# Kernel tuning notes

Measured on AMD Instinct MI355X. Metric: run time of the kernel, lower is better.

## Reference

```python
import jax, jax.numpy as jnp
import numpy as np

WIN = (8, 8)        # window height, width
HEADS = 6
DIM = 192
HEAD_DIM = DIM // HEADS
SCALE = HEAD_DIM ** -0.5
ALPHA = 0.2         # leaky_relu negative slope (tf.nn.leaky_relu / keras default)


def _leaky(t):
    return jnp.where(t >= 0, t, ALPHA * t)


def _relative_position_index():
    # Faithful to the TF code: tf.meshgrid defaults to 'xy' indexing.
    wh, ww = WIN
    mh, mw = jnp.meshgrid(jnp.arange(wh), jnp.arange(ww))  # each [ww, wh] (xy)
    coords = jnp.stack([mh, mw])                           # [2, ww, wh]
    flat = coords.reshape(2, -1)                           # [2, N]
    rel = flat[:, :, None] - flat[:, None, :]              # [2, N, N]
    rel = jnp.transpose(rel, (1, 2, 0))                    # [N, N, 2]
    idx = (rel[:, :, 0] + wh - 1) * (2 * ww - 1) + (rel[:, :, 1] + ww - 1)
    return idx                                             # [N, N] int32


def setup_inputs() -> dict:
    key = jax.random.key(0)
    ks = jax.random.split(key, 6)
    B_, N, C = 4096, WIN[0] * WIN[1], DIM
    std = 0.02
    return {
        "x": jax.random.normal(ks[0], (B_, N, C), dtype=jnp.float32),
        "wq": jax.random.normal(ks[1], (C, C), dtype=jnp.float32) * (C ** -0.5),
        "bq": jnp.zeros((C,), dtype=jnp.float32),
        "wkv": jax.random.normal(ks[2], (C, 2 * C), dtype=jnp.float32) * (C ** -0.5),
        "bkv": jnp.zeros((2 * C,), dtype=jnp.float32),
        "bias_table": jax.random.normal(ks[3], ((2 * WIN[0] - 1) * (2 * WIN[1] - 1), HEADS), dtype=jnp.float32) * std,
        "proj_w": jax.random.normal(ks[4], (C, C), dtype=jnp.float32) * (C ** -0.5),
        "proj_b": jnp.zeros((C,), dtype=jnp.float32),
    }


def reference(x, wq, bq, wkv, bkv, bias_table, proj_w, proj_b):
    B_, N, C = x.shape
    H, D = HEADS, HEAD_DIM

    # QKV projections with LeakyReLU activation (as in LinearProjection)
    q = _leaky(x @ wq + bq).reshape(B_, N, H, D).transpose(0, 2, 1, 3)      # [B,H,N,D]
    kv = _leaky(x @ wkv + bkv).reshape(B_, N, 2, H, D).transpose(2, 0, 3, 1, 4)
    k, v = kv[0], kv[1]                                                      # [B,H,N,D]

    # scaled attention scores
    attn = jnp.einsum('bhnd,bhmd->bhnm', q * SCALE, k)                       # [B,H,N,N]

    # gathered relative position bias (ratio == 1 here, tf.repeat is no-op)
    idx = _relative_position_index()                                         # [N,N]
    bias = bias_table[idx]                                                   # [N,N,H]
    attn = attn + jnp.transpose(bias, (2, 0, 1))[None]                       # [B,H,N,N]

    attn = jax.nn.softmax(attn, axis=-1)
    out = jnp.einsum('bhnm,bhmd->bhnd', attn, v)                             # [B,H,N,D]
    out = out.transpose(0, 2, 1, 3).reshape(B_, N, C)
    return out @ proj_w + proj_b
```

## Files before the change

kernel.cpp:

```cpp
#include <hip/hip_runtime.h>
#include <hip/hip_bf16.h>

typedef __bf16 bf16;
typedef bf16 bf16x8 __attribute__((ext_vector_type(8)));
typedef bf16 bf16x4 __attribute__((ext_vector_type(4)));
typedef short s16x4 __attribute__((ext_vector_type(4)));
typedef float f32x4 __attribute__((ext_vector_type(4)));

#define SCALE 0.17677669529663687f

#define OFF_B 0
#define OFF_K 12800
#define OFF_V 25600
#define SMEM_ELEMS 39424

#if defined(__has_builtin)
#if __has_builtin(__builtin_amdgcn_mfma_f32_16x16x16bf16_1k)
#define HAS_MFMA16 1
#endif
#endif

__global__ void wattn_prep(const float* __restrict__ wq, const float* __restrict__ wkv,
                           const float* __restrict__ bias_table, const float* __restrict__ proj_w,
                           bf16* __restrict__ wqkvT, bf16* __restrict__ projT,
                           float* __restrict__ biasB)
{
    int t = blockIdx.x * 256 + threadIdx.x;
    if (t < 110592) {
        int n = t / 192, k = t % 192;
        float v = (n < 192) ? wq[k * 192 + n] : wkv[k * 384 + (n - 192)];
        wqkvT[t] = (bf16)v;
    } else if (t < 147456) {
        int e = t - 110592;
        int n = e / 192, k = e % 192;
        projT[e] = (bf16)proj_w[k * 192 + n];
    } else if (t < 172032) {
        int e = t - 147456;
        int h  = e >> 12;
        int mb = (e >> 8) & 15;
        int n  = (e >> 2) & 63;
        int mr = e & 3;
        int m  = mb * 4 + mr;
        int idx = ((n & 7) - (m & 7) + 7) * 15 + ((n >> 3) - (m >> 3) + 7);
        biasB[e] = bias_table[idx * 6 + h];
    }
}

__global__ __launch_bounds__(256, 2)
void wattn_main(const float* __restrict__ x, const bf16* __restrict__ wqkvT,
                const float* __restrict__ bq, const float* __restrict__ bkv,
                const bf16* __restrict__ projT, const float* __restrict__ biasB,
                const float* __restrict__ proj_b, float* __restrict__ outg, int B)
{
    __shared__ __align__(16) bf16 smem[SMEM_ELEMS];
    const int tid = threadIdx.x;
    const int li  = tid & 15;
    const int gi  = (tid >> 4) & 3;
    const int w   = tid >> 6;
    const int win = blockIdx.x;
    if (win >= B) return;

    bf16* xq = smem + OFF_B;
    bf16* kb = smem + OFF_K;
    bf16* vt = smem + OFF_V;

    const f32x4 fzero = {0.f, 0.f, 0.f, 0.f};

    {
        const float4* xg = (const float4*)(x + (size_t)win * 12288);
#pragma unroll
        for (int i = 0; i < 12; ++i) {
            float4 p = xg[i * 256 + tid];
            int f = (i * 256 + tid) * 4;
            int r = f / 192, c = f % 192;
            bf16x4 v; v[0]=(bf16)p.x; v[1]=(bf16)p.y; v[2]=(bf16)p.z; v[3]=(bf16)p.w;
            *(bf16x4*)&xq[r * 200 + c] = v;
        }
    }
    __syncthreads();

    f32x4 acc[4][9];
#pragma unroll
    for (int rt = 0; rt < 4; ++rt)
#pragma unroll
        for (int c = 0; c < 9; ++c) acc[rt][c] = fzero;
#pragma unroll
    for (int kk = 0; kk < 6; ++kk) {
        bf16x8 a[4], bw[9];
#pragma unroll
        for (int rt = 0; rt < 4; ++rt)
            a[rt] = *(const bf16x8*)&xq[(rt * 16 + li) * 200 + kk * 32 + gi * 8];
#pragma unroll
        for (int c = 0; c < 9; ++c) {
            int T = w + 4 * c;
            bw[c] = *(const bf16x8*)&wqkvT[(size_t)(T * 16 + li) * 192 + kk * 32 + gi * 8];
        }
#pragma unroll
        for (int c = 0; c < 9; ++c)
#pragma unroll
            for (int rt = 0; rt < 4; ++rt)
                acc[rt][c] = __builtin_amdgcn_mfma_f32_16x16x32_bf16(a[rt], bw[c], acc[rt][c], 0, 0, 0);
    }
    __syncthreads();

#pragma unroll
    for (int c = 0; c < 9; ++c) {
        int T = w + 4 * c;
        int n0 = T * 16;
        float bias = (n0 < 192) ? bq[n0 + li] : bkv[n0 - 192 + li];
#pragma unroll
        for (int rt = 0; rt < 4; ++rt) {
            float vv[4];
#pragma unroll
            for (int rg = 0; rg < 4; ++rg) {
                float v = acc[rt][c][rg] + bias;
                vv[rg] = (v >= 0.f) ? v : 0.2f * v;
            }
            if (T < 12) {
#pragma unroll
                for (int rg = 0; rg < 4; ++rg)
                    xq[(rt * 16 + gi * 4 + rg) * 200 + n0 + li] = (bf16)(vv[rg] * SCALE);
            } else if (T < 24) {
#pragma unroll
                for (int rg = 0; rg < 4; ++rg)
                    kb[(rt * 16 + gi * 4 + rg) * 200 + (n0 - 192) + li] = (bf16)vv[rg];
            } else {
                int cc = n0 - 384;
                int hh = cc >> 5, d0 = cc & 31;
                bf16x4 v4;
#pragma unroll
                for (int rg = 0; rg < 4; ++rg) v4[rg] = (bf16)vv[rg];
                *(bf16x4*)&vt[(hh * 32 + d0 + li) * 72 + rt * 16 + gi * 4] = v4;
            }
        }
    }
    __syncthreads();

    bf16x4 obf[3][2][2];
    for (int jj = 0; jj < 3; ++jj) {
        int job = w * 3 + jj;
        int h   = job >> 1;
        int ct0 = (job & 1) * 2;

        bf16x8 ak[4], bqf[2];
#pragma unroll
        for (int rt = 0; rt < 4; ++rt)
            ak[rt] = *(const bf16x8*)&kb[(rt * 16 + li) * 200 + h * 32 + gi * 8];
#pragma unroll
        for (int c2 = 0; c2 < 2; ++c2)
            bqf[c2] = *(const bf16x8*)&xq[((ct0 + c2) * 16 + li) * 200 + h * 32 + gi * 8];
        f32x4 s[4][2];
#pragma unroll
        for (int rt = 0; rt < 4; ++rt)
#pragma unroll
            for (int c2 = 0; c2 < 2; ++c2)
                s[rt][c2] = __builtin_amdgcn_mfma_f32_16x16x32_bf16(ak[rt], bqf[c2], fzero, 0, 0, 0);
#pragma unroll
        for (int rt = 0; rt < 4; ++rt)
#pragma unroll
            for (int c2 = 0; c2 < 2; ++c2) {
                f32x4 bv = *(const f32x4*)&biasB[h * 4096 + (rt * 4 + gi) * 256 + ((ct0 + c2) * 16 + li) * 4];
                s[rt][c2] += bv;
            }
        float rs[2];
#pragma unroll
        for (int c2 = 0; c2 < 2; ++c2) {
            float m_ = -1e30f;
#pragma unroll
            for (int rt = 0; rt < 4; ++rt)
#pragma unroll
                for (int rg = 0; rg < 4; ++rg) m_ = fmaxf(m_, s[rt][c2][rg]);
            m_ = fmaxf(m_, __shfl_xor(m_, 16));
            m_ = fmaxf(m_, __shfl_xor(m_, 32));
            float ss = 0.f;
#pragma unroll
            for (int rt = 0; rt < 4; ++rt)
#pragma unroll
                for (int rg = 0; rg < 4; ++rg) {
                    float p = __expf(s[rt][c2][rg] - m_);
                    s[rt][c2][rg] = p;
                    ss += p;
                }
            ss += __shfl_xor(ss, 16);
            ss += __shfl_xor(ss, 32);
            rs[c2] = 1.f / ss;
        }

        f32x4 o[2][2];
#pragma unroll
        for (int dt = 0; dt < 2; ++dt)
#pragma unroll
            for (int c2 = 0; c2 < 2; ++c2) o[dt][c2] = fzero;

#if defined(HAS_MFMA16)
#pragma unroll
        for (int ks = 0; ks < 4; ++ks) {
            s16x4 va[2], pb[2];
#pragma unroll
            for (int dt = 0; dt < 2; ++dt)
                va[dt] = *(const s16x4*)&vt[(h * 32 + dt * 16 + li) * 72 + ks * 16 + gi * 4];
#pragma unroll
            for (int c2 = 0; c2 < 2; ++c2) {
                bf16x4 b4;
#pragma unroll
                for (int rg = 0; rg < 4; ++rg) b4[rg] = (bf16)s[ks][c2][rg];
                pb[c2] = __builtin_bit_cast(s16x4, b4);
            }
#pragma unroll
            for (int dt = 0; dt < 2; ++dt)
#pragma unroll
                for (int c2 = 0; c2 < 2; ++c2)
                    o[dt][c2] = __builtin_amdgcn_mfma_f32_16x16x16bf16_1k(va[dt], pb[c2], o[dt][c2], 0, 0, 0);
        }
#else
#pragma unroll
        for (int c2 = 0; c2 < 2; ++c2) {
            unsigned pk[4][2];
#pragma unroll
            for (int rt = 0; rt < 4; ++rt)
#pragma unroll
                for (int pr = 0; pr < 2; ++pr) {
                    bf16 b0 = (bf16)s[rt][c2][2 * pr];
                    bf16 b1 = (bf16)s[rt][c2][2 * pr + 1];
                    unsigned short u0, u1;
                    __builtin_memcpy(&u0, &b0, 2);
                    __builtin_memcpy(&u1, &b1, 2);
                    pk[rt][pr] = (unsigned)u0 | ((unsigned)u1 << 16);
                }
#pragma unroll
            for (int ks = 0; ks < 2; ++ks) {
                union { unsigned u[4]; bf16x8 v; } bu;
#pragma unroll
                for (int p = 0; p < 4; ++p) {
                    int srcLane = li + 16 * (2 * (gi & 1) + (p >> 1));
                    unsigned vA = __shfl(pk[2 * ks][p & 1], srcLane);
                    unsigned vB = __shfl(pk[2 * ks + 1][p & 1], srcLane);
                    bu.u[p] = (gi >> 1) ? vB : vA;
                }
#pragma unroll
                for (int dt = 0; dt < 2; ++dt) {
                    bf16x8 va = *(const bf16x8*)&vt[(h * 32 + dt * 16 + li) * 72 + ks * 32 + gi * 8];
                    o[dt][c2] = __builtin_amdgcn_mfma_f32_16x16x32_bf16(va, bu.v, o[dt][c2], 0, 0, 0);
                }
            }
        }
#endif
#pragma unroll
        for (int dt = 0; dt < 2; ++dt)
#pragma unroll
            for (int c2 = 0; c2 < 2; ++c2) {
                bf16x4 v4;
#pragma unroll
                for (int rg = 0; rg < 4; ++rg) v4[rg] = (bf16)(o[dt][c2][rg] * rs[c2]);
                obf[jj][dt][c2] = v4;
            }
    }
    __syncthreads();

#pragma unroll
    for (int jj = 0; jj < 3; ++jj) {
        int job = w * 3 + jj;
        int h   = job >> 1;
        int ct0 = (job & 1) * 2;
#pragma unroll
        for (int dt = 0; dt < 2; ++dt)
#pragma unroll
            for (int c2 = 0; c2 < 2; ++c2)
                *(bf16x4*)&xq[((ct0 + c2) * 16 + li) * 200 + h * 32 + dt * 16 + gi * 4] = obf[jj][dt][c2];
    }
    __syncthreads();

    f32x4 pacc[4][3];
#pragma unroll
    for (int rt = 0; rt < 4; ++rt)
#pragma unroll
        for (int ct = 0; ct < 3; ++ct) pacc[rt][ct] = fzero;
#pragma unroll
    for (int kk = 0; kk < 6; ++kk) {
        bf16x8 a[4], bw[3];
#pragma unroll
        for (int rt = 0; rt < 4; ++rt)
            a[rt] = *(const bf16x8*)&xq[(rt * 16 + li) * 200 + kk * 32 + gi * 8];
#pragma unroll
        for (int ct = 0; ct < 3; ++ct)
            bw[ct] = *(const bf16x8*)&projT[(size_t)(w * 48 + ct * 16 + li) * 192 + kk * 32 + gi * 8];
#pragma unroll
        for (int ct = 0; ct < 3; ++ct)
#pragma unroll
            for (int rt = 0; rt < 4; ++rt)
                pacc[rt][ct] = __builtin_amdgcn_mfma_f32_16x16x32_bf16(a[rt], bw[ct], pacc[rt][ct], 0, 0, 0);
    }
    {
        float* of = (float*)(smem + OFF_K);
#pragma unroll
        for (int ct = 0; ct < 3; ++ct) {
            int n = w * 48 + ct * 16 + li;
            float pb_ = proj_b[n];
#pragma unroll
            for (int rt = 0; rt < 4; ++rt)
#pragma unroll
                for (int rg = 0; rg < 4; ++rg)
                    of[(rt * 16 + gi * 4 + rg) * 192 + n] = pacc[rt][ct][rg] + pb_;
        }
    }
    __syncthreads();

    {
        const float4* os = (const float4*)(smem + OFF_K);
        float4* og = (float4*)(outg + (size_t)win * 12288);
#pragma unroll
        for (int i = 0; i < 12; ++i)
            og[i * 256 + tid] = os[i * 256 + tid];
    }
}

extern "C" void kernel_launch(void* const* d_in, const int* in_sizes, int n_in,
                              void* d_out, int out_size, void* d_ws, size_t ws_size,
                              hipStream_t stream)
{
    const float* x          = (const float*)d_in[0];
    const float* wq         = (const float*)d_in[1];
    const float* bq         = (const float*)d_in[2];
    const float* wkv        = (const float*)d_in[3];
    const float* bkv        = (const float*)d_in[4];
    const float* bias_table = (const float*)d_in[5];
    const float* proj_w     = (const float*)d_in[6];
    const float* proj_b     = (const float*)d_in[7];
    float* out = (float*)d_out;

    int B = in_sizes[0] / (64 * 192);

    bf16*  wqkvT = (bf16*)d_ws;
    bf16*  projT = (bf16*)((char*)d_ws + 221184);
    float* biasB = (float*)((char*)d_ws + 294912);

    wattn_prep<<<672, 256, 0, stream>>>(wq, wkv, bias_table, proj_w, wqkvT, projT, biasB);

    wattn_main<<<B, 256, 0, stream>>>(x, wqkvT, bq, bkv, projT, biasB, proj_b, out, B);
}
```

Measured before the change: 238.9 us.

## Assign one head per wave with 384-thread blocks and register-resident Q/K

Each block now runs 6 waves, one per attention head. The QKV projection is computed transposed (weights as the A operand), so each wave's Q and K tiles stay in registers and feed the score MFMAs directly. Only V goes to a small per-wave LDS region, which cuts shared memory use and removes two block-wide barriers. The output projection and the coalesced store are also re-split across the 6 waves. The aim is more resident waves and less LDS traffic per window, at the cost of register pressure under the 384-thread, 3-blocks-per-CU launch bounds.

```diff
diff --git a/kernel.cpp b/kernel.cpp
--- a/kernel.cpp
+++ b/kernel.cpp
@@ -9,10 +9,8 @@
 
 #define SCALE 0.17677669529663687f
 
-#define OFF_B 0
-#define OFF_K 12800
-#define OFF_V 25600
-#define SMEM_ELEMS 39424
+#define OFF_V 12800
+#define SMEM_ELEMS 25856
 
 #if defined(__has_builtin)
 #if __has_builtin(__builtin_amdgcn_mfma_f32_16x16x16bf16_1k)
@@ -46,11 +44,28 @@
     }
 }
 
-__global__ __launch_bounds__(256, 2)
+#if !defined(HAS_MFMA16)
+__device__ __forceinline__ bf16x8 build8(bf16x4 t0, bf16x4 t1, int li, int gi) {
+    union { bf16x4 v; unsigned u[2]; } a0, a1;
+    a0.v = t0; a1.v = t1;
+    int b = li + 32 * (gi & 1);
+    unsigned l0  = __shfl(a0.u[0], b),      l1  = __shfl(a0.u[1], b);
+    unsigned l0h = __shfl(a0.u[0], b + 16), l1h = __shfl(a0.u[1], b + 16);
+    unsigned h0  = __shfl(a1.u[0], b),      h1  = __shfl(a1.u[1], b);
+    unsigned h0h = __shfl(a1.u[0], b + 16), h1h = __shfl(a1.u[1], b + 16);
+    bool hi = (gi & 2);
+    union { bf16x8 v8; unsigned u[4]; } r;
+    r.u[0] = hi ? h0 : l0;   r.u[1] = hi ? h1 : l1;
+    r.u[2] = hi ? h0h : l0h; r.u[3] = hi ? h1h : l1h;
+    return r.v8;
+}
+#endif
+
+__global__ __launch_bounds__(384, 3)
 void wattn_main(const float* __restrict__ x, const bf16* __restrict__ wqkvT,
                 const float* __restrict__ bq, const float* __restrict__ bkv,
                 const bf16* __restrict__ projT, const float* __restrict__ biasB,
-                const float* __restrict__ proj_b, float* __restrict__ outg, int B)
+                const float* __restrict__ proj_b, float* __restrict__ outg)
 {
     __shared__ __align__(16) bf16 smem[SMEM_ELEMS];
     const int tid = threadIdx.x;
@@ -58,259 +73,224 @@
     const int gi  = (tid >> 4) & 3;
     const int w   = tid >> 6;
     const int win = blockIdx.x;
-    if (win >= B) return;
-
-    bf16* xq = smem + OFF_B;
-    bf16* kb = smem + OFF_K;
-    bf16* vt = smem + OFF_V;
-
-    const f32x4 fzero = {0.f, 0.f, 0.f, 0.f};
+
+    bf16* xb = smem;
+    bf16* vt = smem + OFF_V + w * 2176;
+
+    const int srow = tid / 48, scol = tid % 48;
+    const f32x4 fz = {0.f, 0.f, 0.f, 0.f};
 
     {
         const float4* xg = (const float4*)(x + (size_t)win * 12288);
 #pragma unroll
-        for (int i = 0; i < 12; ++i) {
-            float4 p = xg[i * 256 + tid];
-            int f = (i * 256 + tid) * 4;
-            int r = f / 192, c = f % 192;
+        for (int i = 0; i < 8; ++i) {
+            float4 p = xg[(srow + 8 * i) * 48 + scol];
             bf16x4 v; v[0]=(bf16)p.x; v[1]=(bf16)p.y; v[2]=(bf16)p.z; v[3]=(bf16)p.w;
-            *(bf16x4*)&xq[r * 200 + c] = v;
-        }
-    }
-    __syncthreads();
-
-    f32x4 acc[4][9];
-#pragma unroll
-    for (int rt = 0; rt < 4; ++rt)
-#pragma unroll
-        for (int c = 0; c < 9; ++c) acc[rt][c] = fzero;
+            *(bf16x4*)&xb[(srow + 8 * i) * 200 + scol * 4] = v;
+        }
+    }
+    __syncthreads();
+
+    f32x4 acc[6][4];
+#pragma unroll
+    for (int j = 0; j < 6; ++j)
+#pragma unroll
+        for (int c = 0; c < 4; ++c) acc[j][c] = fz;
 #pragma unroll
     for (int kk = 0; kk < 6; ++kk) {
-        bf16x8 a[4], bw[9];
-#pragma unroll
-        for (int rt = 0; rt < 4; ++rt)
-            a[rt] = *(const bf16x8*)&xq[(rt * 16 + li) * 200 + kk * 32 + gi * 8];
-#pragma unroll
-        for (int c = 0; c < 9; ++c) {
-            int T = w + 4 * c;
-            bw[c] = *(const bf16x8*)&wqkvT[(size_t)(T * 16 + li) * 192 + kk * 32 + gi * 8];
-        }
-#pragma unroll
-        for (int c = 0; c < 9; ++c)
-#pragma unroll
-            for (int rt = 0; rt < 4; ++rt)
-                acc[rt][c] = __builtin_amdgcn_mfma_f32_16x16x32_bf16(a[rt], bw[c], acc[rt][c], 0, 0, 0);
-    }
-    __syncthreads();
-
-#pragma unroll
-    for (int c = 0; c < 9; ++c) {
-        int T = w + 4 * c;
-        int n0 = T * 16;
-        float bias = (n0 < 192) ? bq[n0 + li] : bkv[n0 - 192 + li];
-#pragma unroll
-        for (int rt = 0; rt < 4; ++rt) {
-            float vv[4];
-#pragma unroll
-            for (int rg = 0; rg < 4; ++rg) {
-                float v = acc[rt][c][rg] + bias;
-                vv[rg] = (v >= 0.f) ? v : 0.2f * v;
-            }
-            if (T < 12) {
-#pragma unroll
-                for (int rg = 0; rg < 4; ++rg)
-                    xq[(rt * 16 + gi * 4 + rg) * 200 + n0 + li] = (bf16)(vv[rg] * SCALE);
-            } else if (T < 24) {
-#pragma unroll
-                for (int rg = 0; rg < 4; ++rg)
-                    kb[(rt * 16 + gi * 4 + rg) * 200 + (n0 - 192) + li] = (bf16)vv[rg];
-            } else {
-                int cc = n0 - 384;
-                int hh = cc >> 5, d0 = cc & 31;
-                bf16x4 v4;
-#pragma unroll
-                for (int rg = 0; rg < 4; ++rg) v4[rg] = (bf16)vv[rg];
-                *(bf16x4*)&vt[(hh * 32 + d0 + li) * 72 + rt * 16 + gi * 4] = v4;
-            }
-        }
-    }
-    __syncthreads();
-
-    bf16x4 obf[3][2][2];
-    for (int jj = 0; jj < 3; ++jj) {
-        int job = w * 3 + jj;
-        int h   = job >> 1;
-        int ct0 = (job & 1) * 2;
-
-        bf16x8 ak[4], bqf[2];
-#pragma unroll
-        for (int rt = 0; rt < 4; ++rt)
-            ak[rt] = *(const bf16x8*)&kb[(rt * 16 + li) * 200 + h * 32 + gi * 8];
-#pragma unroll
-        for (int c2 = 0; c2 < 2; ++c2)
-            bqf[c2] = *(const bf16x8*)&xq[((ct0 + c2) * 16 + li) * 200 + h * 32 + gi * 8];
-        f32x4 s[4][2];
-#pragma unroll
-        for (int rt = 0; rt < 4; ++rt)
-#pragma unroll
-            for (int c2 = 0; c2 < 2; ++c2)
-                s[rt][c2] = __builtin_amdgcn_mfma_f32_16x16x32_bf16(ak[rt], bqf[c2], fzero, 0, 0, 0);
-#pragma unroll
-        for (int rt = 0; rt < 4; ++rt)
-#pragma unroll
-            for (int c2 = 0; c2 < 2; ++c2) {
-                f32x4 bv = *(const f32x4*)&biasB[h * 4096 + (rt * 4 + gi) * 256 + ((ct0 + c2) * 16 + li) * 4];
-                s[rt][c2] += bv;
-            }
-        float rs[2];
-#pragma unroll
-        for (int c2 = 0; c2 < 2; ++c2) {
-            float m_ = -1e30f;
-#pragma unroll
-            for (int rt = 0; rt < 4; ++rt)
-#pragma unroll
-                for (int rg = 0; rg < 4; ++rg) m_ = fmaxf(m_, s[rt][c2][rg]);
-            m_ = fmaxf(m_, __shfl_xor(m_, 16));
-            m_ = fmaxf(m_, __shfl_xor(m_, 32));
-            float ss = 0.f;
-#pragma unroll
-            for (int rt = 0; rt < 4; ++rt)
+        bf16x8 bx[4], aw[6];
+#pragma unroll
+        for (int c = 0; c < 4; ++c)
+            bx[c] = *(const bf16x8*)&xb[(c * 16 + li) * 200 + kk * 32 + gi * 8];
+#pragma unroll
+        for (int j = 0; j < 6; ++j) {
+            int T = (j < 2) ? (2 * w + j) : (j < 4) ? (12 + 2 * w + (j - 2)) : (24 + 2 * w + (j - 4));
+            aw[j] = *(const bf16x8*)&wqkvT[(size_t)(T * 16 + li) * 192 + kk * 32 + gi * 8];
+        }
+#pragma unroll
+        for (int j = 0; j < 6; ++j)
+#pragma unroll
+            for (int c = 0; c < 4; ++c)
+                acc[j][c] = __builtin_amdgcn_mfma_f32_16x16x32_bf16(aw[j], bx[c], acc[j][c], 0, 0, 0);
+    }
+    __syncthreads();
+
+    bf16x4 qf[2][4], kf[2][4];
+    {
+        float4 bb[6];
+#pragma unroll
+        for (int j = 0; j < 2; ++j) bb[j]     = *(const float4*)&bq [32 * w + 16 * j + 4 * gi];
+#pragma unroll
+        for (int j = 0; j < 2; ++j) bb[2 + j] = *(const float4*)&bkv[32 * w + 16 * j + 4 * gi];
+#pragma unroll
+        for (int j = 0; j < 2; ++j) bb[4 + j] = *(const float4*)&bkv[192 + 32 * w + 16 * j + 4 * gi];
+#pragma unroll
+        for (int j = 0; j < 6; ++j) {
+            const float* bp = (const float*)&bb[j];
+#pragma unroll
+            for (int c = 0; c < 4; ++c) {
+                bf16x4 r;
 #pragma unroll
                 for (int rg = 0; rg < 4; ++rg) {
-                    float p = __expf(s[rt][c2][rg] - m_);
-                    s[rt][c2][rg] = p;
-                    ss += p;
+                    float t = acc[j][c][rg] + bp[rg];
+                    t = fmaxf(t, 0.f) + 0.2f * fminf(t, 0.f);
+                    if (j < 2) t *= SCALE;
+                    r[rg] = (bf16)t;
                 }
-            ss += __shfl_xor(ss, 16);
-            ss += __shfl_xor(ss, 32);
-            rs[c2] = 1.f / ss;
-        }
-
-        f32x4 o[2][2];
-#pragma unroll
-        for (int dt = 0; dt < 2; ++dt)
-#pragma unroll
-            for (int c2 = 0; c2 < 2; ++c2) o[dt][c2] = fzero;
-
-#if defined(HAS_MFMA16)
-#pragma unroll
-        for (int ks = 0; ks < 4; ++ks) {
-            s16x4 va[2], pb[2];
-#pragma unroll
-            for (int dt = 0; dt < 2; ++dt)
-                va[dt] = *(const s16x4*)&vt[(h * 32 + dt * 16 + li) * 72 + ks * 16 + gi * 4];
-#pragma unroll
-            for (int c2 = 0; c2 < 2; ++c2) {
-                bf16x4 b4;
-#pragma unroll
-                for (int rg = 0; rg < 4; ++rg) b4[rg] = (bf16)s[ks][c2][rg];
-                pb[c2] = __builtin_bit_cast(s16x4, b4);
-            }
-#pragma unroll
-            for (int dt = 0; dt < 2; ++dt)
-#pragma unroll
-                for (int c2 = 0; c2 < 2; ++c2)
-                    o[dt][c2] = __builtin_amdgcn_mfma_f32_16x16x16bf16_1k(va[dt], pb[c2], o[dt][c2], 0, 0, 0);
-        }
-#else
-#pragma unroll
-        for (int c2 = 0; c2 < 2; ++c2) {
-            unsigned pk[4][2];
-#pragma unroll
-            for (int rt = 0; rt < 4; ++rt)
-#pragma unroll
-                for (int pr = 0; pr < 2; ++pr) {
-                    bf16 b0 = (bf16)s[rt][c2][2 * pr];
-                    bf16 b1 = (bf16)s[rt][c2][2 * pr + 1];
-                    unsigned short u0, u1;
-                    __builtin_memcpy(&u0, &b0, 2);
-                    __builtin_memcpy(&u1, &b1, 2);
-                    pk[rt][pr] = (unsigned)u0 | ((unsigned)u1 << 16);
-                }
-#pragma unroll
-            for (int ks = 0; ks < 2; ++ks) {
-                union { unsigned u[4]; bf16x8 v; } bu;
-#pragma unroll
-                for (int p = 0; p < 4; ++p) {
-                    int srcLane = li + 16 * (2 * (gi & 1) + (p >> 1));
-                    unsigned vA = __shfl(pk[2 * ks][p & 1], srcLane);
-                    unsigned vB = __shfl(pk[2 * ks + 1][p & 1], srcLane);
-                    bu.u[p] = (gi >> 1) ? vB : vA;
-                }
-#pragma unroll
-                for (int dt = 0; dt < 2; ++dt) {
-                    bf16x8 va = *(const bf16x8*)&vt[(h * 32 + dt * 16 + li) * 72 + ks * 32 + gi * 8];
-                    o[dt][c2] = __builtin_amdgcn_mfma_f32_16x16x32_bf16(va, bu.v, o[dt][c2], 0, 0, 0);
+                if (j < 2)      qf[j][c] = r;
+                else if (j < 4) kf[j - 2][c] = r;
+                else {
+#pragma unroll
+                    for (int rg = 0; rg < 4; ++rg)
+                        vt[(16 * (j - 4) + 4 * gi + rg) * 68 + c * 16 + li] = r[rg];
                 }
             }
         }
-#endif
-#pragma unroll
-        for (int dt = 0; dt < 2; ++dt)
-#pragma unroll
-            for (int c2 = 0; c2 < 2; ++c2) {
-                bf16x4 v4;
-#pragma unroll
-                for (int rg = 0; rg < 4; ++rg) v4[rg] = (bf16)(o[dt][c2][rg] * rs[c2]);
-                obf[jj][dt][c2] = v4;
+    }
+
+    f32x4 s[4][4];
+#if defined(HAS_MFMA16)
+#pragma unroll
+    for (int cm = 0; cm < 4; ++cm)
+#pragma unroll
+        for (int cn = 0; cn < 4; ++cn) {
+            f32x4 t = __builtin_amdgcn_mfma_f32_16x16x16bf16_1k(
+                __builtin_bit_cast(s16x4, kf[0][cm]), __builtin_bit_cast(s16x4, qf[0][cn]), fz, 0, 0, 0);
+            s[cm][cn] = __builtin_amdgcn_mfma_f32_16x16x16bf16_1k(
+                __builtin_bit_cast(s16x4, kf[1][cm]), __builtin_bit_cast(s16x4, qf[1][cn]), t, 0, 0, 0);
+        }
+#else
+    {
+        bf16x8 ka[4], qb[4];
+#pragma unroll
+        for (int cm = 0; cm < 4; ++cm) ka[cm] = build8(kf[0][cm], kf[1][cm], li, gi);
+#pragma unroll
+        for (int cn = 0; cn < 4; ++cn) qb[cn] = build8(qf[0][cn], qf[1][cn], li, gi);
+#pragma unroll
+        for (int cm = 0; cm < 4; ++cm)
+#pragma unroll
+            for (int cn = 0; cn < 4; ++cn)
+                s[cm][cn] = __builtin_amdgcn_mfma_f32_16x16x32_bf16(ka[cm], qb[cn], fz, 0, 0, 0);
+    }
+#endif
+
+    float rs[4];
+    bf16x4 pb[4][4];
+#pragma unroll
+    for (int cn = 0; cn < 4; ++cn) {
+        float m_ = -1e30f;
+#pragma unroll
+        for (int cm = 0; cm < 4; ++cm) {
+            s[cm][cn] += *(const f32x4*)&biasB[w * 4096 + (4 * cm + gi) * 256 + (16 * cn + li) * 4];
+#pragma unroll
+            for (int rg = 0; rg < 4; ++rg) m_ = fmaxf(m_, s[cm][cn][rg]);
+        }
+        m_ = fmaxf(m_, __shfl_xor(m_, 16));
+        m_ = fmaxf(m_, __shfl_xor(m_, 32));
+        float ss = 0.f;
+#pragma unroll
+        for (int cm = 0; cm < 4; ++cm) {
+            bf16x4 r;
+#pragma unroll
+            for (int rg = 0; rg < 4; ++rg) {
+                float p = __expf(s[cm][cn][rg] - m_);
+                ss += p;
+                r[rg] = (bf16)p;
             }
-    }
-    __syncthreads();
-
-#pragma unroll
-    for (int jj = 0; jj < 3; ++jj) {
-        int job = w * 3 + jj;
-        int h   = job >> 1;
-        int ct0 = (job & 1) * 2;
-#pragma unroll
-        for (int dt = 0; dt < 2; ++dt)
-#pragma unroll
-            for (int c2 = 0; c2 < 2; ++c2)
-                *(bf16x4*)&xq[((ct0 + c2) * 16 + li) * 200 + h * 32 + dt * 16 + gi * 4] = obf[jj][dt][c2];
-    }
-    __syncthreads();
-
-    f32x4 pacc[4][3];
-#pragma unroll
-    for (int rt = 0; rt < 4; ++rt)
-#pragma unroll
-        for (int ct = 0; ct < 3; ++ct) pacc[rt][ct] = fzero;
+            pb[cm][cn] = r;
+        }
+        ss += __shfl_xor(ss, 16);
+        ss += __shfl_xor(ss, 32);
+        rs[cn] = 1.f / ss;
+    }
+
+    f32x4 o[2][4];
+#pragma unroll
+    for (int dt = 0; dt < 2; ++dt) {
+#if defined(HAS_MFMA16)
+        s16x4 av[4];
+#pragma unroll
+        for (int ks = 0; ks < 4; ++ks)
+            av[ks] = *(const s16x4*)&vt[(dt * 16 + li) * 68 + ks * 16 + gi * 4];
+#pragma unroll
+        for (int cn = 0; cn < 4; ++cn) {
+            f32x4 t = fz;
+#pragma unroll
+            for (int ks = 0; ks < 4; ++ks)
+                t = __builtin_amdgcn_mfma_f32_16x16x16bf16_1k(
+                        av[ks], __builtin_bit_cast(s16x4, pb[ks][cn]), t, 0, 0, 0);
+            o[dt][cn] = t;
+        }
+#else
+        bf16x8 av2[2];
+#pragma unroll
+        for (int c = 0; c < 2; ++c)
+            av2[c] = *(const bf16x8*)&vt[(dt * 16 + li) * 68 + c * 32 + gi * 8];
+#pragma unroll
+        for (int cn = 0; cn < 4; ++cn) {
+            f32x4 t = fz;
+#pragma unroll
+            for (int c = 0; c < 2; ++c)
+                t = __builtin_amdgcn_mfma_f32_16x16x32_bf16(
+                        av2[c], build8(pb[2 * c][cn], pb[2 * c + 1][cn], li, gi), t, 0, 0, 0);
+            o[dt][cn] = t;
+        }
+#endif
+    }
+#pragma unroll
+    for (int dt = 0; dt < 2; ++dt)
+#pragma unroll
+        for (int cn = 0; cn < 4; ++cn) {
+            bf16x4 r;
+#pragma unroll
+            for (int rg = 0; rg < 4; ++rg) r[rg] = (bf16)(o[dt][cn][rg] * rs[cn]);
+            *(bf16x4*)&xb[(cn * 16 + li) * 200 + 32 * w + 16 * dt + 4 * gi] = r;
+        }
+    __syncthreads();
+
+    f32x4 pa[2][4];
+#pragma unroll
+    for (int ct = 0; ct < 2; ++ct)
+#pragma unroll
+        for (int cn = 0; cn < 4; ++cn) pa[ct][cn] = fz;
 #pragma unroll
     for (int kk = 0; kk < 6; ++kk) {
-        bf16x8 a[4], bw[3];
-#pragma unroll
-        for (int rt = 0; rt < 4; ++rt)
-            a[rt] = *(const bf16x8*)&xq[(rt * 16 + li) * 200 + kk * 32 + gi * 8];
-#pragma unroll
-        for (int ct = 0; ct < 3; ++ct)
-            bw[ct] = *(const bf16x8*)&projT[(size_t)(w * 48 + ct * 16 + li) * 192 + kk * 32 + gi * 8];
-#pragma unroll
-        for (int ct = 0; ct < 3; ++ct)
-#pragma unroll
-            for (int rt = 0; rt < 4; ++rt)
-                pacc[rt][ct] = __builtin_amdgcn_mfma_f32_16x16x32_bf16(a[rt], bw[ct], pacc[rt][ct], 0, 0, 0);
-    }
-    {
-        float* of = (float*)(smem + OFF_K);
-#pragma unroll
-        for (int ct = 0; ct < 3; ++ct) {
-            int n = w * 48 + ct * 16 + li;
-            float pb_ = proj_b[n];
-#pragma unroll
-            for (int rt = 0; rt < 4; ++rt)
-#pragma unroll
-                for (int rg = 0; rg < 4; ++rg)
-                    of[(rt * 16 + gi * 4 + rg) * 192 + n] = pacc[rt][ct][rg] + pb_;
-        }
-    }
-    __syncthreads();
-
-    {
-        const float4* os = (const float4*)(smem + OFF_K);
+        bf16x8 bo[4], awp[2];
+#pragma unroll
+        for (int cn = 0; cn < 4; ++cn)
+            bo[cn] = *(const bf16x8*)&xb[(cn * 16 + li) * 200 + kk * 32 + gi * 8];
+#pragma unroll
+        for (int ct = 0; ct < 2; ++ct)
+            awp[ct] = *(const bf16x8*)&projT[(size_t)((2 * w + ct) * 16 + li) * 192 + kk * 32 + gi * 8];
+#pragma unroll
+        for (int ct = 0; ct < 2; ++ct)
+#pragma unroll
+            for (int cn = 0; cn < 4; ++cn)
+                pa[ct][cn] = __builtin_amdgcn_mfma_f32_16x16x32_bf16(awp[ct], bo[cn], pa[ct][cn], 0, 0, 0);
+    }
+    __syncthreads();
+
+    {
+        float* of = (float*)smem;
+#pragma unroll
+        for (int ct = 0; ct < 2; ++ct) {
+            float4 pbv = *(const float4*)&proj_b[32 * w + 16 * ct + 4 * gi];
+#pragma unroll
+            for (int cn = 0; cn < 4; ++cn) {
+                f32x4 y = pa[ct][cn];
+                y[0] += pbv.x; y[1] += pbv.y; y[2] += pbv.z; y[3] += pbv.w;
+                *(f32x4*)&of[(cn * 16 + li) * 200 + 32 * w + 16 * ct + 4 * gi] = y;
+            }
+        }
+    }
+    __syncthreads();
+
+    {
+        const float* ofr = (const float*)smem;
         float4* og = (float4*)(outg + (size_t)win * 12288);
 #pragma unroll
-        for (int i = 0; i < 12; ++i)
-            og[i * 256 + tid] = os[i * 256 + tid];
+        for (int i = 0; i < 8; ++i)
+            og[(srow + 8 * i) * 48 + scol] = *(const float4*)&ofr[(srow + 8 * i) * 200 + scol * 4];
     }
 }
 
@@ -336,5 +316,5 @@
 
     wattn_prep<<<672, 256, 0, stream>>>(wq, wkv, bias_table, proj_w, wqkvT, projT, biasB);
 
-    wattn_main<<<B, 256, 0, stream>>>(x, wqkvT, bq, bkv, projT, biasB, proj_b, out, B);
+    wattn_main<<<B, 384, 0, stream>>>(x, wqkvT, bq, bkv, projT, biasB, proj_b, out);
 }
```

New measurement: 350.3 us. +46.7%, slower.
